# Optimization experiments

Measured on AMD Instinct MI355X. Metric: run time of the kernel, lower is better.

The kernel has to match this reference:

```python
import jax, jax.numpy as jnp
import numpy as np
from jax import lax

LATENT = 128
CODEBOOK = 1024

def _conv(x, w, b):
    # NCHW conv, kernel OIHW, stride 1, padding 1 (same)
    y = lax.conv_general_dilated(x, w, (1, 1), ((1, 1), (1, 1)),
                                 dimension_numbers=('NCHW', 'OIHW', 'NCHW'))
    return y + b[None, :, None, None]

def _conv_transpose(x, w, b):
    # ConvTranspose2d(k=3, s=1, p=1) == conv with flipped kernel, in/out swapped, pad 1
    w_eff = jnp.flip(w, (2, 3)).transpose(1, 0, 2, 3)  # [Cin,Cout,3,3] -> [Cout,Cin,3,3]
    return _conv(x, w_eff, b)

def _maxpool2(x):
    return lax.reduce_window(x, -jnp.inf, lax.max, (1, 1, 2, 2), (1, 1, 2, 2), 'VALID')

def _upsample2(x):
    # F.interpolate(scale_factor=2), default nearest
    return jnp.repeat(jnp.repeat(x, 2, axis=2), 2, axis=3)

def setup_inputs() -> dict:
    key = jax.random.key(0)
    ks = jax.random.split(key, 20)
    f = jnp.float32
    inp = {
        'x': jax.random.uniform(ks[0], (8192, 1, 24, 24), dtype=f),
        'conv1_w': jax.random.normal(ks[1], (32, 1, 3, 3), f) * 0.1,
        'conv1_b': jnp.zeros((32,), f),
        'conv2_w': jax.random.normal(ks[2], (64, 32, 3, 3), f) * 0.05,
        'conv2_b': jnp.zeros((64,), f),
        'conv3_w': jax.random.normal(ks[3], (128, 64, 3, 3), f) * 0.04,
        'conv3_b': jnp.zeros((128,), f),
        'enc_fc_w': jax.random.normal(ks[4], (LATENT, 3 * 3 * 128), f) * 0.03,
        'enc_fc_b': jnp.zeros((LATENT,), f),
        'codebook': jax.random.normal(ks[5], (CODEBOOK, LATENT), f),
        'dec_fc_w': jax.random.normal(ks[6], (3 * 3 * 128, LATENT), f) * 0.09,
        'dec_fc_b': jnp.zeros((3 * 3 * 128,), f),
        'dct1_w': jax.random.normal(ks[7], (128, 64, 3, 3), f) * 0.03,  # [Cin,Cout,kh,kw]
        'dct1_b': jnp.zeros((64,), f),
        'dct2_w': jax.random.normal(ks[8], (64, 32, 3, 3), f) * 0.04,
        'dct2_b': jnp.zeros((32,), f),
        'dct3_w': jax.random.normal(ks[9], (32, 1, 3, 3), f) * 0.06,
        'dct3_b': jnp.zeros((1,), f),
    }
    return inp

def reference(x, conv1_w, conv1_b, conv2_w, conv2_b, conv3_w, conv3_b,
              enc_fc_w, enc_fc_b, codebook, dec_fc_w, dec_fc_b,
              dct1_w, dct1_b, dct2_w, dct2_b, dct3_w, dct3_b):
    # ---- Encoder ----
    h = _maxpool2(jax.nn.relu(_conv(x, conv1_w, conv1_b)))     # [B,32,12,12]
    h = _maxpool2(jax.nn.relu(_conv(h, conv2_w, conv2_b)))     # [B,64,6,6]
    h = _maxpool2(jax.nn.relu(_conv(h, conv3_w, conv3_b)))     # [B,128,3,3]
    z = h.reshape(-1, 3 * 3 * 128) @ enc_fc_w.T + enc_fc_b     # [B,128]
    # ---- Quantize (L2 nearest-codeword; matmul-trick distances, same argmin) ----
    d2 = (jnp.sum(z * z, axis=1, keepdims=True)
          - 2.0 * z @ codebook.T
          + jnp.sum(codebook * codebook, axis=1)[None, :])     # [B,K]
    idx = jnp.argmin(d2, axis=1)                               # [B]
    z_q = codebook[idx]                                        # [B,128]
    # ---- Decoder ----
    d = z_q @ dec_fc_w.T + dec_fc_b                            # [B,1152]
    d = d.reshape(-1, 128, 3, 3)
    d = _upsample2(jax.nn.relu(_conv_transpose(d, dct1_w, dct1_b)))  # [B,64,6,6]
    d = _upsample2(jax.nn.relu(_conv_transpose(d, dct2_w, dct2_b)))  # [B,32,12,12]
    d = _upsample2(jax.nn.relu(_conv_transpose(d, dct3_w, dct3_b)))  # [B,1,24,24]
    return d
```

## Files before the change

### kernel.cpp

```cpp
#include <hip/hip_runtime.h>

typedef __attribute__((ext_vector_type(8))) short short8;
typedef __attribute__((ext_vector_type(4))) float f32x4;
typedef unsigned short ushort_t;
typedef unsigned int uint_t;

#define OFF_W1R   0
#define OFF_W2R   288
#define OFF_W3R   (288+18432)
#define OFF_EWT   (18720+73728)
#define OFF_CT    (92448+147456)
#define OFF_CC    (239904+131072)
#define OFF_DWT   (370976+1024)
#define OFF_D1R   (372000+147456)
#define OFF_D2R   (519456+73728)
#define OFF_D3R   (593184+18432)
#define WS_WEIGHTS (611616+288)
#define OFF_W2BF  WS_WEIGHTS
#define OFF_W3BF  (OFF_W2BF+18432)
#define OFF_H     (OFF_W3BF+73728)
#define OFF_TABLE OFF_H
#define OFF_IDSN  (OFF_H+8192*1152)

__device__ __forceinline__ ushort_t f2bf(float v) {
  uint_t u = __float_as_uint(v);
  return (ushort_t)((u + 0x7FFFu + ((u >> 16) & 1u)) >> 16);
}
__device__ __forceinline__ float bf2f(ushort_t b) {
  return __uint_as_float(((uint_t)b) << 16);
}

__global__ void vq_prep(const float* __restrict__ conv1_w, const float* __restrict__ conv2_w,
                        const float* __restrict__ conv3_w, const float* __restrict__ enc_fc_w,
                        const float* __restrict__ codebook, const float* __restrict__ dec_fc_w,
                        const float* __restrict__ dct1_w, const float* __restrict__ dct2_w,
                        const float* __restrict__ dct3_w, float* __restrict__ ws) {
  int i = blockIdx.x * blockDim.x + threadIdx.x;
  if (i >= WS_WEIGHTS) return;
  if (i < OFF_W2R) {
    int tap = i >> 5, co = i & 31;
    ws[i] = conv1_w[co*9 + tap];
  } else if (i < OFF_W3R) {
    int l = i - OFF_W2R;
    int co = l & 63, r = l >> 6, tap = r % 9, ci = r / 9;
    ws[i] = conv2_w[(co*32 + ci)*9 + tap];
  } else if (i < OFF_EWT) {
    int l = i - OFF_W3R;
    int co = l & 127, r = l >> 7, tap = r % 9, ci = r / 9;
    ws[i] = conv3_w[(co*64 + ci)*9 + tap];
  } else if (i < OFF_CC) {
    return;
  } else if (i < OFF_DWT) {
    int k = i - OFF_CC;
    float s = 0.f;
    for (int j = 0; j < 128; ++j) { float v = codebook[k*128+j]; s += v*v; }
    ws[i] = s;
  } else if (i < OFF_D1R) {
    int l = i - OFF_DWT;
    int j = l % 1152, k = l / 1152;
    ws[i] = dec_fc_w[j*128 + k];
  } else if (i < OFF_D2R) {
    int l = i - OFF_D1R;
    int co = l & 63, r = l >> 6, tap = r % 9, ci = r / 9;
    ws[i] = dct1_w[(ci*64 + co)*9 + (8 - tap)];
  } else if (i < OFF_D3R) {
    int l = i - OFF_D2R;
    int co = l & 31, r = l >> 5, tap = r % 9, ci = r / 9;
    ws[i] = dct2_w[(ci*32 + co)*9 + (8 - tap)];
  } else {
    int l = i - OFF_D3R;
    int tap = l % 9, ci = l / 9;
    ws[i] = dct3_w[ci*9 + (8 - tap)];
  }
}

__global__ void vq_prep2(const float* __restrict__ conv2_w, const float* __restrict__ conv3_w,
                         float* __restrict__ ws) {
  int i = blockIdx.x * blockDim.x + threadIdx.x;
  ushort_t* W2 = (ushort_t*)(ws + OFF_W2BF);
  ushort_t* W3 = (ushort_t*)(ws + OFF_W3BF);
  if (i < 18432) {
    int tap = i >> 11, r = i & 2047, co = r >> 5, ch = r & 31;
    float v = conv2_w[(co*32 + ch)*9 + tap];
    ushort_t hb = f2bf(v);
    W2[i] = hb; W2[18432 + i] = f2bf(v - bf2f(hb));
  } else if (i < 92160) {
    int j = i - 18432;
    int tap = j >> 13, r = j & 8191, co = r >> 6, ch = r & 63;
    float v = conv3_w[(co*64 + ch)*9 + tap];
    ushort_t hb = f2bf(v);
    W3[j] = hb; W3[73728 + j] = f2bf(v - bf2f(hb));
  }
}

__global__ __launch_bounds__(256, 3) void vq_enc(
    const float* __restrict__ x,
    const float* __restrict__ b1, const float* __restrict__ b2, const float* __restrict__ b3,
    const float* __restrict__ ws, float* __restrict__ hout)
{
  __shared__ ushort_t R0h[7840], R0l[7840];
  __shared__ ushort_t C3h[4608], C3l[4608];
  __shared__ float XT[624];
  const int t = threadIdx.x;
  const int b = blockIdx.x;

  for (int i = t; i < 3920; i += 256) { ((uint_t*)R0h)[i] = 0u; ((uint_t*)R0l)[i] = 0u; }
  for (int i = t; i < 2304; i += 256) { ((uint_t*)C3h)[i] = 0u; ((uint_t*)C3l)[i] = 0u; }
  const float* xb = x + (size_t)b * 576;
  for (int i = t; i < 624; i += 256) {
    int row = i / 26, col = i - row * 26;
    XT[i] = (col >= 1 && col <= 24) ? xb[row*24 + col - 1] : 0.f;
  }
  __syncthreads();

  {
    int co = t & 31, g = t >> 5, gy = g >> 1, gx = g & 1;
    float w[9];
    #pragma unroll
    for (int k = 0; k < 9; ++k) w[k] = ws[OFF_W1R + k*32 + co];
    float bias = b1[co];
    #pragma unroll
    for (int pr = 0; pr < 3; ++pr) {
      int Y = gy*6 + pr*2;
      float a0[12], a1[12];
      #pragma unroll
      for (int i = 0; i < 12; ++i) { a0[i] = 0.f; a1[i] = 0.f; }
      #pragma unroll
      for (int wy = 0; wy < 4; ++wy) {
        int ry = Y - 1 + wy;
        if (ry < 0 || ry > 23) continue;
        const float2* rp = (const float2*)&XT[ry*26 + gx*12];
        float r[14];
        #pragma unroll
        for (int k = 0; k < 7; ++k) { float2 p = rp[k]; r[2*k] = p.x; r[2*k+1] = p.y; }
        if (wy < 3) {
          #pragma unroll
          for (int xx = 0; xx < 12; ++xx)
            #pragma unroll
            for (int dx = 0; dx < 3; ++dx) a0[xx] += r[xx+dx] * w[wy*3+dx];
        }
        if (wy >= 1) {
          #pragma unroll
          for (int xx = 0; xx < 12; ++xx)
            #pragma unroll
            for (int dx = 0; dx < 3; ++dx) a1[xx] += r[xx+dx] * w[(wy-1)*3+dx];
        }
      }
      #pragma unroll
      for (int pc = 0; pc < 6; ++pc) {
        float m = fmaxf(fmaxf(a0[2*pc], a0[2*pc+1]), fmaxf(a1[2*pc], a1[2*pc+1]));
        float v = m + bias; v = v > 0.f ? v : 0.f;
        int row = gy*3 + pr, colp = gx*6 + pc;
        int addr = ((row+1)*14 + (colp+1))*40 + co;
        ushort_t hb = f2bf(v);
        R0h[addr] = hb;
        R0l[addr] = f2bf(v - bf2f(hb));
      }
    }
  }
  __syncthreads();

  const int lane = t & 63, quad = lane >> 4, col = lane & 15;
  const int wv = t >> 6;

  {
    const int h = wv & 1, p = wv >> 1;
    const ushort_t* W2 = (const ushort_t*)(ws + OFF_W2BF);
    int baseA[5];
    #pragma unroll
    for (int mi = 0; mi < 5; ++mi) {
      int m = (h*5 + mi)*16 + col; if (m > 143) m = 143;
      int cell = m >> 2, sub = m & 3;
      int opy = cell / 6, opx = cell - opy*6;
      int y = 2*opy + (sub >> 1), xx = 2*opx + (sub & 1);
      baseA[mi] = (y*14 + xx)*40 + quad*8;
    }
    f32x4 acc[5][2];
    #pragma unroll
    for (int mi = 0; mi < 5; ++mi) { acc[mi][0] = (f32x4)0.f; acc[mi][1] = (f32x4)0.f; }
    const int co0 = p*32 + col, co1 = co0 + 16;
    #pragma unroll
    for (int t9 = 0; t9 < 9; ++t9) {
      const int TAPOFF = ((t9/3)*14 + (t9%3))*40;
      int bidx = t9*2048 + quad*8;
      short8 Bh0 = *(const short8*)(W2 + bidx + co0*32);
      short8 Bh1 = *(const short8*)(W2 + bidx + co1*32);
      short8 Bl0 = *(const short8*)(W2 + 18432 + bidx + co0*32);
      short8 Bl1 = *(const short8*)(W2 + 18432 + bidx + co1*32);
      #pragma unroll
      for (int mi = 0; mi < 5; ++mi) {
        int a = baseA[mi] + TAPOFF;
        short8 Ah = *(const short8*)(R0h + a);
        short8 Al = *(const short8*)(R0l + a);
        acc[mi][0] = __builtin_amdgcn_mfma_f32_16x16x32_bf16(Al, Bh0, acc[mi][0], 0, 0, 0);
        acc[mi][0] = __builtin_amdgcn_mfma_f32_16x16x32_bf16(Ah, Bl0, acc[mi][0], 0, 0, 0);
        acc[mi][0] = __builtin_amdgcn_mfma_f32_16x16x32_bf16(Ah, Bh0, acc[mi][0], 0, 0, 0);
        acc[mi][1] = __builtin_amdgcn_mfma_f32_16x16x32_bf16(Al, Bh1, acc[mi][1], 0, 0, 0);
        acc[mi][1] = __builtin_amdgcn_mfma_f32_16x16x32_bf16(Ah, Bl1, acc[mi][1], 0, 0, 0);
        acc[mi][1] = __builtin_amdgcn_mfma_f32_16x16x32_bf16(Ah, Bh1, acc[mi][1], 0, 0, 0);
      }
    }
    #pragma unroll
    for (int mi = 0; mi < 5; ++mi) {
      int cell = (h*5 + mi)*4 + quad;
      if (cell < 36) {
        int opy = cell / 6, opx = cell - opy*6;
        int wa = ((opy+1)*8 + (opx+1))*72;
        #pragma unroll
        for (int j = 0; j < 2; ++j) {
          int ch = j ? co1 : co0;
          f32x4 a = acc[mi][j];
          float v = fmaxf(fmaxf(a.x, a.y), fmaxf(a.z, a.w)) + b2[ch];
          v = v > 0.f ? v : 0.f;
          ushort_t hb = f2bf(v);
          C3h[wa + ch] = hb;
          C3l[wa + ch] = f2bf(v - bf2f(hb));
        }
      }
    }
  }
  __syncthreads();

  {
    const ushort_t* W3 = (const ushort_t*)(ws + OFF_W3BF);
    int baseA[3];
    #pragma unroll
    for (int mt = 0; mt < 3; ++mt) {
      int m = mt*16 + col; if (m > 35) m = 35;
      int cell = m >> 2, sub = m & 3;
      int opy = cell / 3, opx = cell - opy*3;
      int y = 2*opy + (sub >> 1), xx = 2*opx + (sub & 1);
      baseA[mt] = (y*8 + xx)*72 + quad*8;
    }
    f32x4 acc[3][2];
    #pragma unroll
    for (int mt = 0; mt < 3; ++mt) { acc[mt][0] = (f32x4)0.f; acc[mt][1] = (f32x4)0.f; }
    const int co0 = wv*16 + col, co1 = co0 + 64;
    #pragma unroll
    for (int ks = 0; ks < 18; ++ks) {
      const int t9 = ks >> 1, ch0 = (ks & 1)*32;
      const int TAPOFF = ((t9/3)*8 + (t9%3))*72;
      int bidx = t9*8192 + ch0 + quad*8;
      short8 Bh0 = *(const short8*)(W3 + bidx + co0*64);
      short8 Bh1 = *(const short8*)(W3 + bidx + co1*64);
      short8 Bl0 = *(const short8*)(W3 + 73728 + bidx + co0*64);
      short8 Bl1 = *(const short8*)(W3 + 73728 + bidx + co1*64);
      #pragma unroll
      for (int mt = 0; mt < 3; ++mt) {
        int a = baseA[mt] + TAPOFF + ch0;
        short8 Ah = *(const short8*)(C3h + a);
        short8 Al = *(const short8*)(C3l + a);
        acc[mt][0] = __builtin_amdgcn_mfma_f32_16x16x32_bf16(Al, Bh0, acc[mt][0], 0, 0, 0);
        acc[mt][0] = __builtin_amdgcn_mfma_f32_16x16x32_bf16(Ah, Bl0, acc[mt][0], 0, 0, 0);
        acc[mt][0] = __builtin_amdgcn_mfma_f32_16x16x32_bf16(Ah, Bh0, acc[mt][0], 0, 0, 0);
        acc[mt][1] = __builtin_amdgcn_mfma_f32_16x16x32_bf16(Al, Bh1, acc[mt][1], 0, 0, 0);
        acc[mt][1] = __builtin_amdgcn_mfma_f32_16x16x32_bf16(Ah, Bl1, acc[mt][1], 0, 0, 0);
        acc[mt][1] = __builtin_amdgcn_mfma_f32_16x16x32_bf16(Ah, Bh1, acc[mt][1], 0, 0, 0);
      }
    }
    float* hb_ = hout + (size_t)b * 1152;
    #pragma unroll
    for (int mt = 0; mt < 3; ++mt) {
      int cell = mt*4 + quad;
      if (cell < 9) {
        #pragma unroll
        for (int j = 0; j < 2; ++j) {
          int ch = j ? co1 : co0;
          f32x4 a = acc[mt][j];
          float v = fmaxf(fmaxf(a.x, a.y), fmaxf(a.z, a.w)) + b3[ch];
          v = v > 0.f ? v : 0.f;
          hb_[ch*9 + cell] = v;
        }
      }
    }
  }
}

__global__ __launch_bounds__(256, 2) void vq_fc_argmin(
    const float* __restrict__ efw, const float* __restrict__ efb,
    const float* __restrict__ cb, const float* __restrict__ ws,
    const float* __restrict__ h, int* __restrict__ ids)
{
  __shared__ float HT[18432];
  __shared__ float WVs[64];
  __shared__ int   WIs[64];
  const int t = threadIdx.x;
  const int sb = blockIdx.x * 16;

  const float4* src = (const float4*)(h + (size_t)sb * 1152);
  for (int i = t; i < 4608; i += 256) ((float4*)HT)[i] = src[i];
  __syncthreads();

  const int j = t & 127, g = t >> 7;
  float acc[8];
  #pragma unroll
  for (int u = 0; u < 8; ++u) acc[u] = 0.f;
  const float* wj = efw + (size_t)j * 1152;
  for (int k4 = 0; k4 < 1152; k4 += 4) {
    float4 wvv = *(const float4*)(wj + k4);
    const float* hp = &HT[g*9216 + k4];
    #pragma unroll
    for (int u = 0; u < 8; ++u) {
      float4 hv = *(const float4*)(hp + u*1152);
      acc[u] += wvv.x*hv.x + wvv.y*hv.y + wvv.z*hv.z + wvv.w*hv.w;
    }
  }
  float bias = efb[j];
  __syncthreads();
  #pragma unroll
  for (int u = 0; u < 8; ++u) HT[(g*8 + u)*128 + j] = acc[u] + bias;
  __syncthreads();

  float bestv[16]; int besti[16];
  #pragma unroll
  for (int s = 0; s < 16; ++s) { bestv[s] = 3.4e38f; besti[s] = 0; }
  for (int c = 0; c < 4; ++c) {
    int cw = c*256 + t;
    float d[16];
    #pragma unroll
    for (int s = 0; s < 16; ++s) d[s] = 0.f;
    const float* cp = cb + (size_t)cw * 128;
    for (int k4 = 0; k4 < 128; k4 += 4) {
      float4 cv = *(const float4*)(cp + k4);
      #pragma unroll
      for (int s = 0; s < 16; ++s) {
        float4 zv = *(const float4*)(&HT[s*128 + k4]);
        d[s] += cv.x*zv.x + cv.y*zv.y + cv.z*zv.z + cv.w*zv.w;
      }
    }
    float ccv = ws[OFF_CC + cw];
    #pragma unroll
    for (int s = 0; s < 16; ++s) {
      float dist = ccv - 2.f*d[s];
      if (dist < bestv[s]) { bestv[s] = dist; besti[s] = cw; }
    }
  }
  const int lane = t & 63, wid = t >> 6;
  #pragma unroll
  for (int s = 0; s < 16; ++s) {
    float v = bestv[s]; int ii = besti[s];
    #pragma unroll
    for (int off = 32; off >= 1; off >>= 1) {
      float v2 = __shfl_xor(v, off); int i2 = __shfl_xor(ii, off);
      if (v2 < v || (v2 == v && i2 < ii)) { v = v2; ii = i2; }
    }
    if (lane == 0) { WVs[wid*16 + s] = v; WIs[wid*16 + s] = ii; }
  }
  __syncthreads();
  if (t < 16) {
    float v = WVs[t]; int ii = WIs[t];
    #pragma unroll
    for (int w2 = 1; w2 < 4; ++w2) {
      float v2 = WVs[w2*16 + t]; int i2 = WIs[w2*16 + t];
      if (v2 < v || (v2 == v && i2 < ii)) { v = v2; ii = i2; }
    }
    ids[sb + t] = ii;
  }
}

__global__ __launch_bounds__(256, 4) void vq_dec_table(
    const float* __restrict__ codebook, const float* __restrict__ decb,
    const float* __restrict__ d1b, const float* __restrict__ d2b, const float* __restrict__ d3b,
    const float* __restrict__ ws, float* __restrict__ table)
{
  __shared__ float DB[2304];
  __shared__ float R1[2432];
  __shared__ float R0[4736];
  __shared__ float ZQ[256];
  const int t = threadIdx.x;
  const int s0 = blockIdx.x * 2;

  { int s = t >> 7, j = t & 127; ZQ[s*128 + j] = codebook[(size_t)(s0 + s)*128 + j]; }
  __syncthreads();

  #pragma unroll
  for (int p = 0; p < 5; ++p) {
    int j = t + p*256;
    if (j < 1152) {
      float a0 = decb[j], a1 = a0;
      const float* wb = ws + OFF_DWT + j;
      #pragma unroll 4
      for (int k = 0; k < 128; ++k) {
        float wv = wb[k*1152];
        a0 += wv * ZQ[k];
        a1 += wv * ZQ[128 + k];
      }
      DB[j] = a0; DB[1152 + j] = a1;
    }
  }

  for (int s = 0; s < 2; ++s) {
    __syncthreads();
    const float* F = &DB[s*1152];
    float* PS = &DB[s*1152];

    {
      int co = t & 63, g = t >> 6;
      float a9[9];
      #pragma unroll
      for (int i = 0; i < 9; ++i) a9[i] = 0.f;
      const float* wbase = ws + OFF_D1R + co;
      for (int ci = g*32; ci < g*32+32; ++ci) {
        float w[9];
        #pragma unroll
        for (int k = 0; k < 9; ++k) w[k] = wbase[(ci*9+k)*64];
        const float* fin = F + ci*9;
        #pragma unroll
        for (int ry = 0; ry < 3; ++ry) {
          float r[5];
          r[0] = 0.f; r[4] = 0.f;
          r[1] = fin[ry*3]; r[2] = fin[ry*3+1]; r[3] = fin[ry*3+2];
          #pragma unroll
          for (int y = 0; y < 3; ++y) {
            int d = ry - y + 1;
            if (d >= 0 && d < 3) {
              #pragma unroll
              for (int xx = 0; xx < 3; ++xx)
                #pragma unroll
                for (int dx = 0; dx < 3; ++dx) a9[y*3+xx] += r[xx+dx] * w[d*3+dx];
            }
          }
        }
      }
      __syncthreads();
      if (g) {
        #pragma unroll
        for (int i = 0; i < 9; ++i) R0[((g-1)*64 + co)*9 + i] = a9[i];
      }
      __syncthreads();
      if (!g) {
        float bias = d1b[co];
        #pragma unroll
        for (int i = 0; i < 9; ++i)
          a9[i] += R0[co*9 + i] + R0[(64+co)*9 + i] + R0[(128+co)*9 + i];
        #pragma unroll
        for (int yy = 0; yy < 3; ++yy)
          #pragma unroll
          for (int xx = 0; xx < 3; ++xx) {
            float v = a9[yy*3+xx] + bias; v = v > 0.f ? v : 0.f;
            int base = co*38 + (2*yy)*6 + 2*xx;
            R1[base] = v; R1[base+1] = v; R1[base+6] = v; R1[base+7] = v;
          }
      }
    }
    __syncthreads();

    {
      int co = t & 31, hh = (t >> 5) & 1, g = t >> 6;
      int sy = g >> 1, sx = g & 1;
      float a9[9];
      #pragma unroll
      for (int i = 0; i < 9; ++i) a9[i] = 0.f;
      const float* wbase = ws + OFF_D2R + co;
      for (int ci = hh*32; ci < hh*32+32; ++ci) {
        float w[9];
        #pragma unroll
        for (int k = 0; k < 9; ++k) w[k] = wbase[(ci*9+k)*32];
        const float* base = &R1[ci*38];
        #pragma unroll
        for (int wy = 0; wy < 5; ++wy) {
          int ry = sy*3 - 1 + wy;
          if (ry < 0 || ry > 5) continue;
          const float* row = base + ry*6 + sx*3;
          float r[5];
          if (sx == 0) {
            r[0] = 0.f; r[1] = row[0]; r[2] = row[1]; r[3] = row[2]; r[4] = row[3];
          } else {
            r[0] = row[-1]; r[1] = row[0]; r[2] = row[1]; r[3] = row[2]; r[4] = 0.f;
          }
          #pragma unroll
          for (int y = 0; y < 3; ++y) {
            int d = wy - 1 - y + 1;
            if (d >= 0 && d < 3) {
              #pragma unroll
              for (int xx = 0; xx < 3; ++xx)
                #pragma unroll
                for (int dx = 0; dx < 3; ++dx) a9[y*3+xx] += r[xx+dx] * w[d*3+dx];
            }
          }
        }
      }
      __syncthreads();
      if (hh) {
        #pragma unroll
        for (int i = 0; i < 9; ++i) PS[(g*32 + co)*9 + i] = a9[i];
      }
      __syncthreads();
      if (!hh) {
        float bias = d2b[co];
        #pragma unroll
        for (int i = 0; i < 9; ++i) a9[i] += PS[(g*32 + co)*9 + i];
        #pragma unroll
        for (int yy = 0; yy < 3; ++yy)
          #pragma unroll
          for (int xx = 0; xx < 3; ++xx) {
            float v = a9[yy*3+xx] + bias; v = v > 0.f ? v : 0.f;
            int rr = sy*3 + yy, cc_ = sx*3 + xx;
            int base = co*146 + (2*rr)*12 + 2*cc_;
            R0[base] = v; R0[base+1] = v; R0[base+12] = v; R0[base+13] = v;
          }
      }
    }
    __syncthreads();

    if (t < 144) {
      int yy = t / 12, xx = t - yy*12;
      const float* w3 = ws + OFF_D3R;
      float acc = d3b[0];
      for (int ci = 0; ci < 32; ++ci) {
        const float* base = &R0[ci*146];
        #pragma unroll
        for (int dy = 0; dy < 3; ++dy) {
          int ry = yy - 1 + dy;
          int ryc = ry < 0 ? 0 : (ry > 11 ? 11 : ry);
          bool rok = (ry >= 0 && ry < 12);
          #pragma unroll
          for (int dx = 0; dx < 3; ++dx) {
            int rx = xx - 1 + dx;
            int rxc = rx < 0 ? 0 : (rx > 11 ? 11 : rx);
            float v = base[ryc*12 + rxc];
            v = (rok && rx >= 0 && rx < 12) ? v : 0.f;
            acc += v * w3[ci*9 + dy*3 + dx];
          }
        }
      }
      float v = acc > 0.f ? acc : 0.f;
      float* ob = table + (size_t)(s0 + s) * 576;
      int o0 = (2*yy)*24 + 2*xx;
      ob[o0] = v; ob[o0+1] = v; ob[o0+24] = v; ob[o0+25] = v;
    }
  }
}

__global__ __launch_bounds__(256, 8) void vq_scatter(
    const float* __restrict__ table, const int* __restrict__ ids,
    float* __restrict__ out, int nvec)
{
  int idx = blockIdx.x * 256 + threadIdx.x;
  if (idx >= nvec) return;
  int b = idx / 144;
  int r = idx - b * 144;
  int cw = ids[b];
  ((float4*)out)[idx] = ((const float4*)(table + (size_t)cw * 576))[r];
}

extern "C" void kernel_launch(void* const* d_in, const int* in_sizes, int n_in,
                              void* d_out, int out_size, void* d_ws, size_t ws_size,
                              hipStream_t stream) {
  const float* x   = (const float*)d_in[0];
  const float* c1w = (const float*)d_in[1];
  const float* c1b = (const float*)d_in[2];
  const float* c2w = (const float*)d_in[3];
  const float* c2b = (const float*)d_in[4];
  const float* c3w = (const float*)d_in[5];
  const float* c3b = (const float*)d_in[6];
  const float* efw = (const float*)d_in[7];
  const float* efb = (const float*)d_in[8];
  const float* cb  = (const float*)d_in[9];
  const float* dfw = (const float*)d_in[10];
  const float* dfb = (const float*)d_in[11];
  const float* dw1 = (const float*)d_in[12];
  const float* db1 = (const float*)d_in[13];
  const float* dw2 = (const float*)d_in[14];
  const float* db2 = (const float*)d_in[15];
  const float* dw3 = (const float*)d_in[16];
  const float* db3 = (const float*)d_in[17];
  float* ws = (float*)d_ws;
  float* h     = ws + OFF_H;
  float* table = ws + OFF_TABLE;
  int*   ids   = (int*)(ws + OFF_IDSN);
  float* outp = (float*)d_out;
  int B = in_sizes[0] / 576;

  vq_prep<<<(WS_WEIGHTS + 255) / 256, 256, 0, stream>>>(c1w, c2w, c3w, efw, cb, dfw, dw1, dw2, dw3, ws);
  vq_prep2<<<(92160 + 255) / 256, 256, 0, stream>>>(c2w, c3w, ws);
  vq_enc<<<B, 256, 0, stream>>>(x, c1b, c2b, c3b, ws, h);
  vq_fc_argmin<<<B/16, 256, 0, stream>>>(efw, efb, cb, ws, h, ids);
  vq_dec_table<<<512, 256, 0, stream>>>(cb, dfb, db1, db2, db3, ws, table);
  int nvec = B * 144;
  vq_scatter<<<(nvec + 255) / 256, 256, 0, stream>>>(table, ids, outp, nvec);
}
```

Before: 728.3 us.

## Re-layout encoder LDS activations into channel-group planes and retile conv2/conv3 MFMA

The encoder's padded bf16 hi/lo activation buffers move from pixel-major with a 40/72 channel stride to channel-group-major planes of 8 channels. This shrinks LDS use and is meant to cut bank conflicts on the short8 A-operand loads. Conv1 now has each thread produce two channels and write packed 32-bit pairs. Conv2 is retiled so each wave covers up to 3 M-tiles across all 4 N-tiles, with wave 0 taking an extra tile, which reuses each A load across more MFMAs but leaves the work unbalanced. The decoder table kernel now handles one codeword per block over 1024 blocks instead of two per block, and the unused fp32 conv2/conv3 reorder in prep is dropped.

```diff
diff --git a/kernel.cpp b/kernel.cpp
--- a/kernel.cpp
+++ b/kernel.cpp
@@ -30,9 +30,8 @@
   return __uint_as_float(((uint_t)b) << 16);
 }
 
-__global__ void vq_prep(const float* __restrict__ conv1_w, const float* __restrict__ conv2_w,
-                        const float* __restrict__ conv3_w, const float* __restrict__ enc_fc_w,
-                        const float* __restrict__ codebook, const float* __restrict__ dec_fc_w,
+__global__ void vq_prep(const float* __restrict__ conv1_w, const float* __restrict__ codebook,
+                        const float* __restrict__ dec_fc_w,
                         const float* __restrict__ dct1_w, const float* __restrict__ dct2_w,
                         const float* __restrict__ dct3_w, float* __restrict__ ws) {
   int i = blockIdx.x * blockDim.x + threadIdx.x;
@@ -40,14 +39,6 @@
   if (i < OFF_W2R) {
     int tap = i >> 5, co = i & 31;
     ws[i] = conv1_w[co*9 + tap];
-  } else if (i < OFF_W3R) {
-    int l = i - OFF_W2R;
-    int co = l & 63, r = l >> 6, tap = r % 9, ci = r / 9;
-    ws[i] = conv2_w[(co*32 + ci)*9 + tap];
-  } else if (i < OFF_EWT) {
-    int l = i - OFF_W3R;
-    int co = l & 127, r = l >> 7, tap = r % 9, ci = r / 9;
-    ws[i] = conv3_w[(co*64 + ci)*9 + tap];
   } else if (i < OFF_CC) {
     return;
   } else if (i < OFF_DWT) {
@@ -98,123 +89,147 @@
     const float* __restrict__ b1, const float* __restrict__ b2, const float* __restrict__ b3,
     const float* __restrict__ ws, float* __restrict__ hout)
 {
-  __shared__ ushort_t R0h[7840], R0l[7840];
-  __shared__ ushort_t C3h[4608], C3l[4608];
+  __shared__ ushort_t R0h[6272], R0l[6272];
+  __shared__ ushort_t A2h[5120], A2l[5120];
   __shared__ float XT[624];
   const int t = threadIdx.x;
   const int b = blockIdx.x;
 
-  for (int i = t; i < 3920; i += 256) { ((uint_t*)R0h)[i] = 0u; ((uint_t*)R0l)[i] = 0u; }
-  for (int i = t; i < 2304; i += 256) { ((uint_t*)C3h)[i] = 0u; ((uint_t*)C3l)[i] = 0u; }
+  for (int i = t; i < 3136; i += 256) { ((uint_t*)R0h)[i] = 0u; ((uint_t*)R0l)[i] = 0u; }
+  for (int i = t; i < 2560; i += 256) { ((uint_t*)A2h)[i] = 0u; ((uint_t*)A2l)[i] = 0u; }
   const float* xb = x + (size_t)b * 576;
   for (int i = t; i < 624; i += 256) {
-    int row = i / 26, col = i - row * 26;
-    XT[i] = (col >= 1 && col <= 24) ? xb[row*24 + col - 1] : 0.f;
+    int row = i / 26, c = i - row * 26;
+    XT[i] = (c >= 1 && c <= 24) ? xb[row*24 + c - 1] : 0.f;
   }
   __syncthreads();
 
   {
-    int co = t & 31, g = t >> 5, gy = g >> 1, gx = g & 1;
-    float w[9];
-    #pragma unroll
-    for (int k = 0; k < 9; ++k) w[k] = ws[OFF_W1R + k*32 + co];
-    float bias = b1[co];
+    int cp = t & 15, g = t >> 4;
+    int gy = g >> 2, gx = g & 3;
+    float wgt[2][9], bs[2];
+    #pragma unroll
+    for (int c = 0; c < 2; ++c) {
+      bs[c] = b1[2*cp + c];
+      #pragma unroll
+      for (int k = 0; k < 9; ++k) wgt[c][k] = ws[OFF_W1R + k*32 + 2*cp + c];
+    }
+    int quadc = cp >> 2, coff = (cp & 3) * 2;
     #pragma unroll
     for (int pr = 0; pr < 3; ++pr) {
-      int Y = gy*6 + pr*2;
-      float a0[12], a1[12];
-      #pragma unroll
-      for (int i = 0; i < 12; ++i) { a0[i] = 0.f; a1[i] = 0.f; }
+      int Y = (gy*3 + pr)*2;
+      float a0[2][6], a1[2][6];
+      #pragma unroll
+      for (int c = 0; c < 2; ++c)
+        #pragma unroll
+        for (int i = 0; i < 6; ++i) { a0[c][i] = 0.f; a1[c][i] = 0.f; }
       #pragma unroll
       for (int wy = 0; wy < 4; ++wy) {
         int ry = Y - 1 + wy;
         if (ry < 0 || ry > 23) continue;
-        const float2* rp = (const float2*)&XT[ry*26 + gx*12];
-        float r[14];
-        #pragma unroll
-        for (int k = 0; k < 7; ++k) { float2 p = rp[k]; r[2*k] = p.x; r[2*k+1] = p.y; }
+        const float2* rp = (const float2*)&XT[ry*26 + gx*6];
+        float r[8];
+        #pragma unroll
+        for (int k = 0; k < 4; ++k) { float2 p = rp[k]; r[2*k] = p.x; r[2*k+1] = p.y; }
         if (wy < 3) {
           #pragma unroll
-          for (int xx = 0; xx < 12; ++xx)
+          for (int c = 0; c < 2; ++c)
             #pragma unroll
-            for (int dx = 0; dx < 3; ++dx) a0[xx] += r[xx+dx] * w[wy*3+dx];
+            for (int xx = 0; xx < 6; ++xx)
+              #pragma unroll
+              for (int dx = 0; dx < 3; ++dx) a0[c][xx] += r[xx+dx] * wgt[c][wy*3+dx];
         }
         if (wy >= 1) {
           #pragma unroll
-          for (int xx = 0; xx < 12; ++xx)
+          for (int c = 0; c < 2; ++c)
             #pragma unroll
-            for (int dx = 0; dx < 3; ++dx) a1[xx] += r[xx+dx] * w[(wy-1)*3+dx];
-        }
-      }
-      #pragma unroll
-      for (int pc = 0; pc < 6; ++pc) {
-        float m = fmaxf(fmaxf(a0[2*pc], a0[2*pc+1]), fmaxf(a1[2*pc], a1[2*pc+1]));
-        float v = m + bias; v = v > 0.f ? v : 0.f;
-        int row = gy*3 + pr, colp = gx*6 + pc;
-        int addr = ((row+1)*14 + (colp+1))*40 + co;
-        ushort_t hb = f2bf(v);
-        R0h[addr] = hb;
-        R0l[addr] = f2bf(v - bf2f(hb));
-      }
-    }
-  }
-  __syncthreads();
-
-  const int lane = t & 63, quad = lane >> 4, col = lane & 15;
-  const int wv = t >> 6;
+            for (int xx = 0; xx < 6; ++xx)
+              #pragma unroll
+              for (int dx = 0; dx < 3; ++dx) a1[c][xx] += r[xx+dx] * wgt[c][(wy-1)*3+dx];
+        }
+      }
+      #pragma unroll
+      for (int pc = 0; pc < 3; ++pc) {
+        uint_t hi = 0, lo = 0;
+        #pragma unroll
+        for (int c = 0; c < 2; ++c) {
+          float m = fmaxf(fmaxf(a0[c][2*pc], a0[c][2*pc+1]), fmaxf(a1[c][2*pc], a1[c][2*pc+1]));
+          float v = m + bs[c]; v = v > 0.f ? v : 0.f;
+          ushort_t hb = f2bf(v);
+          ushort_t lb = f2bf(v - bf2f(hb));
+          hi |= ((uint_t)hb) << (16*c);
+          lo |= ((uint_t)lb) << (16*c);
+        }
+        int p = (gy*3 + pr + 1)*14 + (gx*3 + pc + 1);
+        int base = quadc*1568 + p*8 + coff;
+        ((uint_t*)R0h)[base >> 1] = hi;
+        ((uint_t*)R0l)[base >> 1] = lo;
+      }
+    }
+  }
+  __syncthreads();
+
+  const int lane = t & 63, wv = t >> 6;
+  const int col = lane & 15, quad = lane >> 4;
 
   {
-    const int h = wv & 1, p = wv >> 1;
     const ushort_t* W2 = (const ushort_t*)(ws + OFF_W2BF);
-    int baseA[5];
-    #pragma unroll
-    for (int mi = 0; mi < 5; ++mi) {
-      int m = (h*5 + mi)*16 + col; if (m > 143) m = 143;
-      int cell = m >> 2, sub = m & 3;
-      int opy = cell / 6, opx = cell - opy*6;
-      int y = 2*opy + (sub >> 1), xx = 2*opx + (sub & 1);
-      baseA[mi] = (y*14 + xx)*40 + quad*8;
-    }
-    f32x4 acc[5][2];
-    #pragma unroll
-    for (int mi = 0; mi < 5; ++mi) { acc[mi][0] = (f32x4)0.f; acc[mi][1] = (f32x4)0.f; }
-    const int co0 = p*32 + col, co1 = co0 + 16;
+    const int mtb = (wv == 0) ? 0 : (wv == 1) ? 3 : (wv == 2) ? 5 : 7;
+    const int cnt = (wv == 0) ? 3 : 2;
+    int pA[3];
+    #pragma unroll
+    for (int mi = 0; mi < 3; ++mi) {
+      int mt = mtb + (mi < cnt ? mi : 0);
+      int cell = mt*4 + (col >> 2), sub = col & 3;
+      int y = 2*(cell/6) + (sub >> 1), xx = 2*(cell%6) + (sub & 1);
+      pA[mi] = y*14 + xx;
+    }
+    f32x4 acc[3][4];
+    #pragma unroll
+    for (int mi = 0; mi < 3; ++mi)
+      #pragma unroll
+      for (int nt = 0; nt < 4; ++nt) acc[mi][nt] = (f32x4)0.f;
     #pragma unroll
     for (int t9 = 0; t9 < 9; ++t9) {
-      const int TAPOFF = ((t9/3)*14 + (t9%3))*40;
-      int bidx = t9*2048 + quad*8;
-      short8 Bh0 = *(const short8*)(W2 + bidx + co0*32);
-      short8 Bh1 = *(const short8*)(W2 + bidx + co1*32);
-      short8 Bl0 = *(const short8*)(W2 + 18432 + bidx + co0*32);
-      short8 Bl1 = *(const short8*)(W2 + 18432 + bidx + co1*32);
-      #pragma unroll
-      for (int mi = 0; mi < 5; ++mi) {
-        int a = baseA[mi] + TAPOFF;
-        short8 Ah = *(const short8*)(R0h + a);
-        short8 Al = *(const short8*)(R0l + a);
-        acc[mi][0] = __builtin_amdgcn_mfma_f32_16x16x32_bf16(Al, Bh0, acc[mi][0], 0, 0, 0);
-        acc[mi][0] = __builtin_amdgcn_mfma_f32_16x16x32_bf16(Ah, Bl0, acc[mi][0], 0, 0, 0);
-        acc[mi][0] = __builtin_amdgcn_mfma_f32_16x16x32_bf16(Ah, Bh0, acc[mi][0], 0, 0, 0);
-        acc[mi][1] = __builtin_amdgcn_mfma_f32_16x16x32_bf16(Al, Bh1, acc[mi][1], 0, 0, 0);
-        acc[mi][1] = __builtin_amdgcn_mfma_f32_16x16x32_bf16(Ah, Bl1, acc[mi][1], 0, 0, 0);
-        acc[mi][1] = __builtin_amdgcn_mfma_f32_16x16x32_bf16(Ah, Bh1, acc[mi][1], 0, 0, 0);
-      }
-    }
-    #pragma unroll
-    for (int mi = 0; mi < 5; ++mi) {
-      int cell = (h*5 + mi)*4 + quad;
-      if (cell < 36) {
-        int opy = cell / 6, opx = cell - opy*6;
-        int wa = ((opy+1)*8 + (opx+1))*72;
-        #pragma unroll
-        for (int j = 0; j < 2; ++j) {
-          int ch = j ? co1 : co0;
-          f32x4 a = acc[mi][j];
+      const int toff = (t9/3)*14 + (t9%3);
+      short8 Bh[4], Bl[4];
+      #pragma unroll
+      for (int nt = 0; nt < 4; ++nt) {
+        int co = nt*16 + col;
+        Bh[nt] = *(const short8*)(W2 + t9*2048 + co*32 + quad*8);
+        Bl[nt] = *(const short8*)(W2 + 18432 + t9*2048 + co*32 + quad*8);
+      }
+      #pragma unroll
+      for (int mi = 0; mi < 3; ++mi) {
+        if (mi < cnt) {
+          int a = quad*1568 + (pA[mi] + toff)*8;
+          short8 Ah = *(const short8*)(R0h + a);
+          short8 Al = *(const short8*)(R0l + a);
+          #pragma unroll
+          for (int nt = 0; nt < 4; ++nt) {
+            acc[mi][nt] = __builtin_amdgcn_mfma_f32_16x16x32_bf16(Al, Bh[nt], acc[mi][nt], 0,0,0);
+            acc[mi][nt] = __builtin_amdgcn_mfma_f32_16x16x32_bf16(Ah, Bl[nt], acc[mi][nt], 0,0,0);
+            acc[mi][nt] = __builtin_amdgcn_mfma_f32_16x16x32_bf16(Ah, Bh[nt], acc[mi][nt], 0,0,0);
+          }
+        }
+      }
+    }
+    #pragma unroll
+    for (int mi = 0; mi < 3; ++mi) {
+      if (mi < cnt) {
+        int mt = mtb + mi;
+        int cell = mt*4 + quad;
+        int p2 = ((cell/6) + 1)*10 + (cell%6) + 1;
+        #pragma unroll
+        for (int nt = 0; nt < 4; ++nt) {
+          int ch = nt*16 + col;
+          f32x4 a = acc[mi][nt];
           float v = fmaxf(fmaxf(a.x, a.y), fmaxf(a.z, a.w)) + b2[ch];
           v = v > 0.f ? v : 0.f;
           ushort_t hb = f2bf(v);
-          C3h[wa + ch] = hb;
-          C3l[wa + ch] = f2bf(v - bf2f(hb));
+          int wa = (ch >> 3)*640 + p2*8 + (ch & 7);
+          A2h[wa] = hb;
+          A2l[wa] = f2bf(v - bf2f(hb));
         }
       }
     }
@@ -223,39 +238,42 @@
 
   {
     const ushort_t* W3 = (const ushort_t*)(ws + OFF_W3BF);
-    int baseA[3];
+    int pA[3];
     #pragma unroll
     for (int mt = 0; mt < 3; ++mt) {
-      int m = mt*16 + col; if (m > 35) m = 35;
-      int cell = m >> 2, sub = m & 3;
-      int opy = cell / 3, opx = cell - opy*3;
-      int y = 2*opy + (sub >> 1), xx = 2*opx + (sub & 1);
-      baseA[mt] = (y*8 + xx)*72 + quad*8;
+      int cell = mt*4 + (col >> 2);
+      if (cell > 8) cell = 8;
+      int sub = col & 3;
+      int y = 2*(cell/3) + (sub >> 1), xx = 2*(cell%3) + (sub & 1);
+      pA[mt] = y*10 + xx;
     }
     f32x4 acc[3][2];
     #pragma unroll
     for (int mt = 0; mt < 3; ++mt) { acc[mt][0] = (f32x4)0.f; acc[mt][1] = (f32x4)0.f; }
-    const int co0 = wv*16 + col, co1 = co0 + 64;
     #pragma unroll
     for (int ks = 0; ks < 18; ++ks) {
-      const int t9 = ks >> 1, ch0 = (ks & 1)*32;
-      const int TAPOFF = ((t9/3)*8 + (t9%3))*72;
-      int bidx = t9*8192 + ch0 + quad*8;
-      short8 Bh0 = *(const short8*)(W3 + bidx + co0*64);
-      short8 Bh1 = *(const short8*)(W3 + bidx + co1*64);
-      short8 Bl0 = *(const short8*)(W3 + 73728 + bidx + co0*64);
-      short8 Bl1 = *(const short8*)(W3 + 73728 + bidx + co1*64);
+      const int t9 = ks >> 1, half = ks & 1;
+      const int toff = (t9/3)*10 + (t9%3);
+      const int grp = half*4 + quad;
+      short8 Bh[2], Bl[2];
+      #pragma unroll
+      for (int j = 0; j < 2; ++j) {
+        int co = (wv*2 + j)*16 + col;
+        int bo = t9*8192 + co*64 + half*32 + quad*8;
+        Bh[j] = *(const short8*)(W3 + bo);
+        Bl[j] = *(const short8*)(W3 + 73728 + bo);
+      }
       #pragma unroll
       for (int mt = 0; mt < 3; ++mt) {
-        int a = baseA[mt] + TAPOFF + ch0;
-        short8 Ah = *(const short8*)(C3h + a);
-        short8 Al = *(const short8*)(C3l + a);
-        acc[mt][0] = __builtin_amdgcn_mfma_f32_16x16x32_bf16(Al, Bh0, acc[mt][0], 0, 0, 0);
-        acc[mt][0] = __builtin_amdgcn_mfma_f32_16x16x32_bf16(Ah, Bl0, acc[mt][0], 0, 0, 0);
-        acc[mt][0] = __builtin_amdgcn_mfma_f32_16x16x32_bf16(Ah, Bh0, acc[mt][0], 0, 0, 0);
-        acc[mt][1] = __builtin_amdgcn_mfma_f32_16x16x32_bf16(Al, Bh1, acc[mt][1], 0, 0, 0);
-        acc[mt][1] = __builtin_amdgcn_mfma_f32_16x16x32_bf16(Ah, Bl1, acc[mt][1], 0, 0, 0);
-        acc[mt][1] = __builtin_amdgcn_mfma_f32_16x16x32_bf16(Ah, Bh1, acc[mt][1], 0, 0, 0);
+        int a = grp*640 + (pA[mt] + toff)*8;
+        short8 Ah = *(const short8*)(A2h + a);
+        short8 Al = *(const short8*)(A2l + a);
+        #pragma unroll
+        for (int j = 0; j < 2; ++j) {
+          acc[mt][j] = __builtin_amdgcn_mfma_f32_16x16x32_bf16(Al, Bh[j], acc[mt][j], 0,0,0);
+          acc[mt][j] = __builtin_amdgcn_mfma_f32_16x16x32_bf16(Ah, Bl[j], acc[mt][j], 0,0,0);
+          acc[mt][j] = __builtin_amdgcn_mfma_f32_16x16x32_bf16(Ah, Bh[j], acc[mt][j], 0,0,0);
+        }
       }
     }
     float* hb_ = hout + (size_t)b * 1152;
@@ -265,7 +283,7 @@
       if (cell < 9) {
         #pragma unroll
         for (int j = 0; j < 2; ++j) {
-          int ch = j ? co1 : co0;
+          int ch = (wv*2 + j)*16 + col;
           f32x4 a = acc[mt][j];
           float v = fmaxf(fmaxf(a.x, a.y), fmaxf(a.z, a.w)) + b3[ch];
           v = v > 0.f ? v : 0.f;
@@ -363,172 +381,163 @@
     const float* __restrict__ d1b, const float* __restrict__ d2b, const float* __restrict__ d3b,
     const float* __restrict__ ws, float* __restrict__ table)
 {
-  __shared__ float DB[2304];
+  __shared__ float DB[1152];
   __shared__ float R1[2432];
   __shared__ float R0[4736];
-  __shared__ float ZQ[256];
+  __shared__ float ZQ[128];
   const int t = threadIdx.x;
-  const int s0 = blockIdx.x * 2;
-
-  { int s = t >> 7, j = t & 127; ZQ[s*128 + j] = codebook[(size_t)(s0 + s)*128 + j]; }
+  const int cw = blockIdx.x;
+
+  if (t < 128) ZQ[t] = codebook[(size_t)cw*128 + t];
   __syncthreads();
 
   #pragma unroll
   for (int p = 0; p < 5; ++p) {
     int j = t + p*256;
     if (j < 1152) {
-      float a0 = decb[j], a1 = a0;
+      float a0 = decb[j];
       const float* wb = ws + OFF_DWT + j;
       #pragma unroll 4
-      for (int k = 0; k < 128; ++k) {
-        float wv = wb[k*1152];
-        a0 += wv * ZQ[k];
-        a1 += wv * ZQ[128 + k];
-      }
-      DB[j] = a0; DB[1152 + j] = a1;
-    }
-  }
-
-  for (int s = 0; s < 2; ++s) {
+      for (int k = 0; k < 128; ++k) a0 += wb[k*1152] * ZQ[k];
+      DB[j] = a0;
+    }
+  }
+  __syncthreads();
+
+  {
+    int co = t & 63, g = t >> 6;
+    float a9[9];
+    #pragma unroll
+    for (int i = 0; i < 9; ++i) a9[i] = 0.f;
+    const float* wbase = ws + OFF_D1R + co;
+    for (int ci = g*32; ci < g*32+32; ++ci) {
+      float w[9];
+      #pragma unroll
+      for (int k = 0; k < 9; ++k) w[k] = wbase[(ci*9+k)*64];
+      const float* fin = DB + ci*9;
+      #pragma unroll
+      for (int ry = 0; ry < 3; ++ry) {
+        float r[5];
+        r[0] = 0.f; r[4] = 0.f;
+        r[1] = fin[ry*3]; r[2] = fin[ry*3+1]; r[3] = fin[ry*3+2];
+        #pragma unroll
+        for (int y = 0; y < 3; ++y) {
+          int d = ry - y + 1;
+          if (d >= 0 && d < 3) {
+            #pragma unroll
+            for (int xx = 0; xx < 3; ++xx)
+              #pragma unroll
+              for (int dx = 0; dx < 3; ++dx) a9[y*3+xx] += r[xx+dx] * w[d*3+dx];
+          }
+        }
+      }
+    }
     __syncthreads();
-    const float* F = &DB[s*1152];
-    float* PS = &DB[s*1152];
-
-    {
-      int co = t & 63, g = t >> 6;
-      float a9[9];
-      #pragma unroll
-      for (int i = 0; i < 9; ++i) a9[i] = 0.f;
-      const float* wbase = ws + OFF_D1R + co;
-      for (int ci = g*32; ci < g*32+32; ++ci) {
-        float w[9];
-        #pragma unroll
-        for (int k = 0; k < 9; ++k) w[k] = wbase[(ci*9+k)*64];
-        const float* fin = F + ci*9;
-        #pragma unroll
-        for (int ry = 0; ry < 3; ++ry) {
-          float r[5];
-          r[0] = 0.f; r[4] = 0.f;
-          r[1] = fin[ry*3]; r[2] = fin[ry*3+1]; r[3] = fin[ry*3+2];
-          #pragma unroll
-          for (int y = 0; y < 3; ++y) {
-            int d = ry - y + 1;
-            if (d >= 0 && d < 3) {
+    if (g) {
+      #pragma unroll
+      for (int i = 0; i < 9; ++i) R0[((g-1)*64 + co)*9 + i] = a9[i];
+    }
+    __syncthreads();
+    if (!g) {
+      float bias = d1b[co];
+      #pragma unroll
+      for (int i = 0; i < 9; ++i)
+        a9[i] += R0[co*9 + i] + R0[(64+co)*9 + i] + R0[(128+co)*9 + i];
+      #pragma unroll
+      for (int yy = 0; yy < 3; ++yy)
+        #pragma unroll
+        for (int xx = 0; xx < 3; ++xx) {
+          float v = a9[yy*3+xx] + bias; v = v > 0.f ? v : 0.f;
+          int base = co*38 + (2*yy)*6 + 2*xx;
+          R1[base] = v; R1[base+1] = v; R1[base+6] = v; R1[base+7] = v;
+        }
+    }
+  }
+  __syncthreads();
+
+  {
+    int co = t & 31, hh = (t >> 5) & 1, g = t >> 6;
+    int sy = g >> 1, sx = g & 1;
+    float a9[9];
+    #pragma unroll
+    for (int i = 0; i < 9; ++i) a9[i] = 0.f;
+    const float* wbase = ws + OFF_D2R + co;
+    for (int ci = hh*32; ci < hh*32+32; ++ci) {
+      float w[9];
+      #pragma unroll
+      for (int k = 0; k < 9; ++k) w[k] = wbase[(ci*9+k)*32];
+      const float* base = &R1[ci*38];
+      #pragma unroll
+      for (int wy = 0; wy < 5; ++wy) {
+        int ry = sy*3 - 1 + wy;
+        if (ry < 0 || ry > 5) continue;
+        const float* row = base + ry*6 + sx*3;
+        float r[5];
+        if (sx == 0) {
+          r[0] = 0.f; r[1] = row[0]; r[2] = row[1]; r[3] = row[2]; r[4] = row[3];
+        } else {
+          r[0] = row[-1]; r[1] = row[0]; r[2] = row[1]; r[3] = row[2]; r[4] = 0.f;
+        }
+        #pragma unroll
+        for (int y = 0; y < 3; ++y) {
+          int d = wy - 1 - y + 1;
+          if (d >= 0 && d < 3) {
+            #pragma unroll
+            for (int xx = 0; xx < 3; ++xx)
               #pragma unroll
-              for (int xx = 0; xx < 3; ++xx)
-                #pragma unroll
-                for (int dx = 0; dx < 3; ++dx) a9[y*3+xx] += r[xx+dx] * w[d*3+dx];
-            }
+              for (int dx = 0; dx < 3; ++dx) a9[y*3+xx] += r[xx+dx] * w[d*3+dx];
           }
         }
       }
-      __syncthreads();
-      if (g) {
-        #pragma unroll
-        for (int i = 0; i < 9; ++i) R0[((g-1)*64 + co)*9 + i] = a9[i];
-      }
-      __syncthreads();
-      if (!g) {
-        float bias = d1b[co];
-        #pragma unroll
-        for (int i = 0; i < 9; ++i)
-          a9[i] += R0[co*9 + i] + R0[(64+co)*9 + i] + R0[(128+co)*9 + i];
-        #pragma unroll
-        for (int yy = 0; yy < 3; ++yy)
-          #pragma unroll
-          for (int xx = 0; xx < 3; ++xx) {
-            float v = a9[yy*3+xx] + bias; v = v > 0.f ? v : 0.f;
-            int base = co*38 + (2*yy)*6 + 2*xx;
-            R1[base] = v; R1[base+1] = v; R1[base+6] = v; R1[base+7] = v;
-          }
-      }
     }
     __syncthreads();
-
-    {
-      int co = t & 31, hh = (t >> 5) & 1, g = t >> 6;
-      int sy = g >> 1, sx = g & 1;
-      float a9[9];
-      #pragma unroll
-      for (int i = 0; i < 9; ++i) a9[i] = 0.f;
-      const float* wbase = ws + OFF_D2R + co;
-      for (int ci = hh*32; ci < hh*32+32; ++ci) {
-        float w[9];
-        #pragma unroll
-        for (int k = 0; k < 9; ++k) w[k] = wbase[(ci*9+k)*32];
-        const float* base = &R1[ci*38];
-        #pragma unroll
-        for (int wy = 0; wy < 5; ++wy) {
-          int ry = sy*3 - 1 + wy;
-          if (ry < 0 || ry > 5) continue;
-          const float* row = base + ry*6 + sx*3;
-          float r[5];
-          if (sx == 0) {
-            r[0] = 0.f; r[1] = row[0]; r[2] = row[1]; r[3] = row[2]; r[4] = row[3];
-          } else {
-            r[0] = row[-1]; r[1] = row[0]; r[2] = row[1]; r[3] = row[2]; r[4] = 0.f;
-          }
-          #pragma unroll
-          for (int y = 0; y < 3; ++y) {
-            int d = wy - 1 - y + 1;
-            if (d >= 0 && d < 3) {
-              #pragma unroll
-              for (int xx = 0; xx < 3; ++xx)
-                #pragma unroll
-                for (int dx = 0; dx < 3; ++dx) a9[y*3+xx] += r[xx+dx] * w[d*3+dx];
-            }
-          }
-        }
-      }
-      __syncthreads();
-      if (hh) {
-        #pragma unroll
-        for (int i = 0; i < 9; ++i) PS[(g*32 + co)*9 + i] = a9[i];
-      }
-      __syncthreads();
-      if (!hh) {
-        float bias = d2b[co];
-        #pragma unroll
-        for (int i = 0; i < 9; ++i) a9[i] += PS[(g*32 + co)*9 + i];
-        #pragma unroll
-        for (int yy = 0; yy < 3; ++yy)
-          #pragma unroll
-          for (int xx = 0; xx < 3; ++xx) {
-            float v = a9[yy*3+xx] + bias; v = v > 0.f ? v : 0.f;
-            int rr = sy*3 + yy, cc_ = sx*3 + xx;
-            int base = co*146 + (2*rr)*12 + 2*cc_;
-            R0[base] = v; R0[base+1] = v; R0[base+12] = v; R0[base+13] = v;
-          }
-      }
+    if (hh) {
+      #pragma unroll
+      for (int i = 0; i < 9; ++i) DB[(g*32 + co)*9 + i] = a9[i];
     }
     __syncthreads();
-
-    if (t < 144) {
-      int yy = t / 12, xx = t - yy*12;
-      const float* w3 = ws + OFF_D3R;
-      float acc = d3b[0];
-      for (int ci = 0; ci < 32; ++ci) {
-        const float* base = &R0[ci*146];
-        #pragma unroll
-        for (int dy = 0; dy < 3; ++dy) {
-          int ry = yy - 1 + dy;
-          int ryc = ry < 0 ? 0 : (ry > 11 ? 11 : ry);
-          bool rok = (ry >= 0 && ry < 12);
-          #pragma unroll
-          for (int dx = 0; dx < 3; ++dx) {
-            int rx = xx - 1 + dx;
-            int rxc = rx < 0 ? 0 : (rx > 11 ? 11 : rx);
-            float v = base[ryc*12 + rxc];
-            v = (rok && rx >= 0 && rx < 12) ? v : 0.f;
-            acc += v * w3[ci*9 + dy*3 + dx];
-          }
-        }
-      }
-      float v = acc > 0.f ? acc : 0.f;
-      float* ob = table + (size_t)(s0 + s) * 576;
-      int o0 = (2*yy)*24 + 2*xx;
-      ob[o0] = v; ob[o0+1] = v; ob[o0+24] = v; ob[o0+25] = v;
-    }
+    if (!hh) {
+      float bias = d2b[co];
+      #pragma unroll
+      for (int i = 0; i < 9; ++i) a9[i] += DB[(g*32 + co)*9 + i];
+      #pragma unroll
+      for (int yy = 0; yy < 3; ++yy)
+        #pragma unroll
+        for (int xx = 0; xx < 3; ++xx) {
+          float v = a9[yy*3+xx] + bias; v = v > 0.f ? v : 0.f;
+          int rr = sy*3 + yy, cc_ = sx*3 + xx;
+          int base = co*146 + (2*rr)*12 + 2*cc_;
+          R0[base] = v; R0[base+1] = v; R0[base+12] = v; R0[base+13] = v;
+        }
+    }
+  }
+  __syncthreads();
+
+  if (t < 144) {
+    int yy = t / 12, xx = t - yy*12;
+    const float* w3 = ws + OFF_D3R;
+    float acc = d3b[0];
+    for (int ci = 0; ci < 32; ++ci) {
+      const float* base = &R0[ci*146];
+      #pragma unroll
+      for (int dy = 0; dy < 3; ++dy) {
+        int ry = yy - 1 + dy;
+        int ryc = ry < 0 ? 0 : (ry > 11 ? 11 : ry);
+        bool rok = (ry >= 0 && ry < 12);
+        #pragma unroll
+        for (int dx = 0; dx < 3; ++dx) {
+          int rx = xx - 1 + dx;
+          int rxc = rx < 0 ? 0 : (rx > 11 ? 11 : rx);
+          float v = base[ryc*12 + rxc];
+          v = (rok && rx >= 0 && rx < 12) ? v : 0.f;
+          acc += v * w3[ci*9 + dy*3 + dx];
+        }
+      }
+    }
+    float v = acc > 0.f ? acc : 0.f;
+    float* ob = table + (size_t)cw * 576;
+    int o0 = (2*yy)*24 + 2*xx;
+    ob[o0] = v; ob[o0+1] = v; ob[o0+24] = v; ob[o0+25] = v;
   }
 }
 
@@ -572,11 +581,11 @@
   float* outp = (float*)d_out;
   int B = in_sizes[0] / 576;
 
-  vq_prep<<<(WS_WEIGHTS + 255) / 256, 256, 0, stream>>>(c1w, c2w, c3w, efw, cb, dfw, dw1, dw2, dw3, ws);
+  vq_prep<<<(WS_WEIGHTS + 255) / 256, 256, 0, stream>>>(c1w, cb, dfw, dw1, dw2, dw3, ws);
   vq_prep2<<<(92160 + 255) / 256, 256, 0, stream>>>(c2w, c3w, ws);
   vq_enc<<<B, 256, 0, stream>>>(x, c1b, c2b, c3b, ws, h);
   vq_fc_argmin<<<B/16, 256, 0, stream>>>(efw, efb, cb, ws, h, ids);
-  vq_dec_table<<<512, 256, 0, stream>>>(cb, dfb, db1, db2, db3, ws, table);
+  vq_dec_table<<<1024, 256, 0, stream>>>(cb, dfb, db1, db2, db3, ws, table);
   int nvec = B * 144;
   vq_scatter<<<(nvec + 255) / 256, 256, 0, stream>>>(table, ids, outp, nvec);
 }
```

Measured after the change: 788.9 us. 8.3% more time.
